# Performance work log

Measured on AMD Instinct MI355X. Metric: run time of the kernel, lower is better.

The kernel has to match this reference:

```python
import jax, jax.numpy as jnp
import numpy as np

B, T, C_EMB, HEAD = 8, 2048, 1024, 64

def setup_inputs() -> dict:
    key = jax.random.key(0)
    kx, kq, kk, kv = jax.random.split(key, 4)
    x = jax.random.normal(kx, (B, T, C_EMB), dtype=jnp.float32)
    s = 1.0 / np.sqrt(C_EMB)
    Wq = jax.random.normal(kq, (C_EMB, HEAD), dtype=jnp.float32) * s
    Wk = jax.random.normal(kk, (C_EMB, HEAD), dtype=jnp.float32) * s
    Wv = jax.random.normal(kv, (C_EMB, HEAD), dtype=jnp.float32) * s
    return {"x": x, "Wq": Wq, "Wk": Wk, "Wv": Wv}


def _apply_rotary(q, k):
    # q, k: [B, T, D] with D = head_size; matches torch apply_rotary_emb
    D = q.shape[-1]
    pos = jnp.arange(q.shape[1], dtype=jnp.float32)                # [T]
    dim_arr = jnp.arange(0, D, 2, dtype=jnp.float32)               # [D/2]
    freqs = 10000.0 ** (-dim_arr / D)                              # [D/2]
    theta = pos[:, None] * freqs[None, :]                          # [T, D/2]
    cos = jnp.concatenate([jnp.cos(theta), jnp.cos(theta)], -1)[None]  # [1,T,D]
    sin = jnp.concatenate([jnp.sin(theta), jnp.sin(theta)], -1)[None]

    def rot(v):
        v1, v2 = v[..., : D // 2], v[..., D // 2 :]
        return jnp.concatenate([-v2, v1], axis=-1)

    return q * cos + rot(q) * sin, k * cos + rot(k) * sin


def reference(x, Wq, Wk, Wv):
    Bx, Tx, Cx = x.shape
    q = x @ Wq  # [B,T,H]
    k = x @ Wk
    v = x @ Wv
    q, k = _apply_rotary(q, k)
    # NOTE: original scales by C**-0.5 where C = n_embd, not head_size
    scale = Cx ** (-0.5)
    wei = jnp.einsum("bqd,bkd->bqk", q, k) * scale                 # [B,T,T]
    causal = jnp.tril(jnp.ones((Tx, Tx), dtype=bool))
    wei = jnp.where(causal[None], wei, -jnp.inf)
    wei = jax.nn.softmax(wei, axis=-1)
    out = jnp.einsum("bqk,bkd->bqd", wei, v)                       # [B,T,H]
    return out
```

## Files before the change

kernel.cpp:

```cpp
#include <hip/hip_runtime.h>

typedef __bf16 bf16x8 __attribute__((ext_vector_type(8)));
typedef float f32x4 __attribute__((ext_vector_type(4)));
typedef unsigned short u16;

#define MFMA __builtin_amdgcn_mfma_f32_16x16x32_bf16

__device__ __forceinline__ u16 f2bf_bits(float f) {
  unsigned u = __builtin_bit_cast(unsigned, f);
  u = (u + 0x7fffu + ((u >> 16) & 1u)) >> 16;
  return (u16)u;
}
__device__ __forceinline__ __bf16 f2bf(float f) {
  u16 b = f2bf_bits(f);
  return __builtin_bit_cast(__bf16, b);
}
__device__ __forceinline__ float bf2f(u16 b) {
  return __builtin_bit_cast(float, (unsigned)b << 16);
}

__device__ __forceinline__ int swz_off(int row, int col) {
  return row * 64 + ((((col >> 3) ^ row) & 7) << 3) + (col & 7);
}
__device__ __forceinline__ bf16x8 lds_read8(const __bf16* buf, int row, int col) {
  return *(const bf16x8*)(buf + (row * 64 + ((((col >> 3) ^ row) & 7) << 3)));
}
__device__ __forceinline__ void lds_write8(__bf16* buf, int row, int col, bf16x8 v) {
  *(bf16x8*)(buf + (row * 64 + ((((col >> 3) ^ row) & 7) << 3))) = v;
}

__global__ __launch_bounds__(256) void prep_w_kernel(
    const float* __restrict__ Wq, const float* __restrict__ Wk,
    const float* __restrict__ Wv, u16* __restrict__ wtg) {
  int idx = blockIdx.x * 256 + threadIdx.x;
  if (idx >= 192 * 1024) return;
  int row = idx >> 10, k = idx & 1023;
  const float* W = (row < 64) ? Wq : ((row < 128) ? Wk : Wv);
  int col = row & 63;
  wtg[idx] = f2bf_bits(W[(size_t)k * 64 + col]);
}

__device__ __forceinline__ void rope2(f32x4& lo, f32x4& hi, int i, float t_base) {
  float f = __expf(-(float)i * 0.28782313662425572f);
  const float inv2pi = 0.15915494309189535f;
#pragma unroll
  for (int r = 0; r < 4; ++r) {
    float rev = (t_base + (float)r) * f * inv2pi;
    rev = __builtin_amdgcn_fractf(rev);
    float sn = __builtin_amdgcn_sinf(rev);
    float cs = __builtin_amdgcn_cosf(rev);
    float L = lo[r], H = hi[r];
    lo[r] = L * cs - H * sn;
    hi[r] = H * cs + L * sn;
  }
}

__global__ __launch_bounds__(512) void qkv_rope_kernel(
    const float* __restrict__ x, const u16* __restrict__ wtg,
    u16* __restrict__ qg, u16* __restrict__ kg, u16* __restrict__ vtg) {
  __shared__ __bf16 xbuf[2][64 * 64];
  __shared__ __bf16 wbuf[2][192 * 64];
  const int tid = threadIdx.x;
  const int w = tid >> 6, l = tid & 63;
  const int wrg = w & 1;
  const int wcg = w >> 1;
  const int lr = l & 15, lg = l >> 4;
  const int r0 = blockIdx.x * 64;
  const int b = r0 >> 11, t0 = r0 & 2047;
  constexpr int TM4[4][3] = {{0, 2, 8}, {1, 3, 9}, {4, 6, 10}, {5, 7, 11}};

  f32x4 acc[2][3];
#pragma unroll
  for (int rg = 0; rg < 2; ++rg)
#pragma unroll
    for (int j = 0; j < 3; ++j) acc[rg][j] = (f32x4){0.f, 0.f, 0.f, 0.f};

  const int srow = tid >> 3, sc8 = tid & 7;
  const float* xbase = x + (size_t)(r0 + srow) * 1024 + sc8 * 8;

  float4 xA0, xA1, xB0, xB1;
  bf16x8 swr[3];

  auto loadW = [&](int k0) {
#pragma unroll
    for (int s = 0; s < 3; ++s) {
      int id = tid + s * 512;
      swr[s] = *(const bf16x8*)(wtg + (size_t)(id >> 3) * 1024 + k0 + (id & 7) * 8);
    }
  };
  auto writeW = [&](int bsel) {
#pragma unroll
    for (int s = 0; s < 3; ++s) {
      int id = tid + s * 512;
      lds_write8(wbuf[bsel], id >> 3, (id & 7) * 8, swr[s]);
    }
  };
  auto writeX = [&](int bsel, float4 a0, float4 a1) {
    bf16x8 v;
    v[0] = f2bf(a0.x); v[1] = f2bf(a0.y); v[2] = f2bf(a0.z); v[3] = f2bf(a0.w);
    v[4] = f2bf(a1.x); v[5] = f2bf(a1.y); v[6] = f2bf(a1.z); v[7] = f2bf(a1.w);
    lds_write8(xbuf[bsel], srow, sc8 * 8, v);
  };

  xA0 = *(const float4*)xbase;
  xA1 = *(const float4*)(xbase + 4);
  loadW(0);
  writeX(0, xA0, xA1);
  writeW(0);
  xB0 = *(const float4*)(xbase + 64);
  xB1 = *(const float4*)(xbase + 68);
  __syncthreads();

#pragma unroll
  for (int s = 0; s < 16; ++s) {
    const int cur = s & 1;
    if (s < 14) {
      const float* p = xbase + (size_t)(s + 2) * 64;
      if (cur == 0) { xA0 = *(const float4*)p; xA1 = *(const float4*)(p + 4); }
      else          { xB0 = *(const float4*)p; xB1 = *(const float4*)(p + 4); }
    }
    if (s < 15) loadW((s + 1) * 64);
#pragma unroll
    for (int kk = 0; kk < 2; ++kk) {
      bf16x8 a0 = lds_read8(xbuf[cur], wrg * 32 + lr, kk * 32 + lg * 8);
      bf16x8 a1 = lds_read8(xbuf[cur], wrg * 32 + 16 + lr, kk * 32 + lg * 8);
#pragma unroll
      for (int j = 0; j < 3; ++j) {
        bf16x8 bb = lds_read8(wbuf[cur], TM4[wcg][j] * 16 + lr, kk * 32 + lg * 8);
        acc[0][j] = MFMA(a0, bb, acc[0][j], 0, 0, 0);
        acc[1][j] = MFMA(a1, bb, acc[1][j], 0, 0, 0);
      }
    }
    if (s < 15) {
      if (cur == 0) writeX(1, xB0, xB1);
      else          writeX(0, xA0, xA1);
      writeW(cur ^ 1);
      __syncthreads();
    }
  }

  const int ph = (wcg & 1) * 16 + lr;
#pragma unroll
  for (int rg = 0; rg < 2; ++rg) {
    const int rowb = wrg * 32 + rg * 16 + lg * 4;
    const float t_base = (float)(t0 + rowb);
    rope2(acc[rg][0], acc[rg][1], ph, t_base);
    if (wcg < 2) {
#pragma unroll
      for (int r = 0; r < 4; ++r) {
        size_t rowo = (size_t)(r0 + rowb + r) * 64;
        qg[rowo + ph] = f2bf_bits(acc[rg][0][r] * 0.03125f);
        qg[rowo + 32 + ph] = f2bf_bits(acc[rg][1][r] * 0.03125f);
      }
    } else {
#pragma unroll
      for (int r = 0; r < 4; ++r) {
        size_t rowo = (size_t)(r0 + rowb + r) * 64;
        kg[rowo + ph] = f2bf_bits(acc[rg][0][r]);
        kg[rowo + 32 + ph] = f2bf_bits(acc[rg][1][r]);
      }
    }
    {
      const int d = (TM4[wcg][2] - 8) * 16 + lr;
      ushort4 uv;
      uv.x = f2bf_bits(acc[rg][2][0]);
      uv.y = f2bf_bits(acc[rg][2][1]);
      uv.z = f2bf_bits(acc[rg][2][2]);
      uv.w = f2bf_bits(acc[rg][2][3]);
      *(ushort4*)(vtg + (size_t)(b * 64 + d) * 2048 + t0 + rowb) = uv;
    }
  }
}

__global__ __launch_bounds__(256) void attn_part_kernel(
    const u16* __restrict__ qg, const u16* __restrict__ kg,
    const u16* __restrict__ vtg, u16* __restrict__ opart,
    float* __restrict__ lpart, float* __restrict__ out, int CT, int NCH) {
  const int idx = blockIdx.x;
  const int b = idx / (32 * NCH);
  const int rem = idx % (32 * NCH);
  const int qt = rem / NCH, ch = rem % NCH;
  const int t0v = ch * CT;
  if (t0v > qt) return;
  const int t1v = min(qt + 1, t0v + CT);
  const int nv = qt / CT + 1;

  __shared__ __bf16 kbuf[2][64 * 64];
  __shared__ __bf16 vbuf[2][64 * 64];
  __shared__ __bf16 pbuf[4 * 16 * 64];
  const int tid = threadIdx.x;
  const int w = tid >> 6, l = tid & 63;
  const int lr = l & 15, lg = l >> 4;
  const int q0 = qt * 64;
  const float NEG_INF = -__builtin_inff();

  const u16* qrow = qg + (size_t)(b * 2048 + q0 + w * 16 + lr) * 64;
  bf16x8 qf0 = *(const bf16x8*)(qrow + lg * 8);
  bf16x8 qf1 = *(const bf16x8*)(qrow + 32 + lg * 8);

  bf16x8 kr[2], vr[2];
  auto stage_load = [&](int c) {
#pragma unroll
    for (int s = 0; s < 2; ++s) {
      int id = tid + s * 256;
      int row = id >> 3, c8 = id & 7;
      kr[s] = *(const bf16x8*)(kg + (size_t)(b * 2048 + c * 64 + row) * 64 + c8 * 8);
      vr[s] = *(const bf16x8*)(vtg + (size_t)(b * 64 + row) * 2048 + c * 64 + c8 * 8);
    }
  };
  auto stage_write = [&](int bsel) {
#pragma unroll
    for (int s = 0; s < 2; ++s) {
      int id = tid + s * 256;
      int row = id >> 3, c8 = id & 7;
      lds_write8(kbuf[bsel], row, c8 * 8, kr[s]);
      lds_write8(vbuf[bsel], row, c8 * 8, vr[s]);
    }
  };

  f32x4 acc_o[4];
#pragma unroll
  for (int n = 0; n < 4; ++n) acc_o[n] = (f32x4){0.f, 0.f, 0.f, 0.f};
  float l_p[4] = {0.f, 0.f, 0.f, 0.f};

  stage_load(t0v);
  stage_write(0);
  __syncthreads();

  for (int c = t0v; c < t1v; ++c) {
    const int cur = (c - t0v) & 1;
    const bool more = (c + 1 < t1v);
    if (more) stage_load(c + 1);

    f32x4 s4[4];
#pragma unroll
    for (int nt = 0; nt < 4; ++nt) {
      bf16x8 k0 = lds_read8(kbuf[cur], nt * 16 + lr, lg * 8);
      bf16x8 k1 = lds_read8(kbuf[cur], nt * 16 + lr, 32 + lg * 8);
      f32x4 t = (f32x4){0.f, 0.f, 0.f, 0.f};
      t = MFMA(qf0, k0, t, 0, 0, 0);
      t = MFMA(qf1, k1, t, 0, 0, 0);
      s4[nt] = t;
    }
    if (c == qt) {
#pragma unroll
      for (int nt = 0; nt < 4; ++nt)
#pragma unroll
        for (int r = 0; r < 4; ++r) {
          int kv = nt * 16 + lr, qq = w * 16 + lg * 4 + r;
          if (kv > qq) s4[nt][r] = NEG_INF;
        }
    }
    __bf16* pw = pbuf + w * (16 * 64);
#pragma unroll
    for (int nt = 0; nt < 4; ++nt)
#pragma unroll
      for (int r = 0; r < 4; ++r) {
        float p = __expf(s4[nt][r] - 8.0f);
        l_p[r] += p;
        pw[swz_off(lg * 4 + r, nt * 16 + lr)] = f2bf(p);
      }
#pragma unroll
    for (int h = 0; h < 2; ++h) {
      bf16x8 pf = lds_read8(pw, lr, h * 32 + lg * 8);
#pragma unroll
      for (int nt = 0; nt < 4; ++nt) {
        bf16x8 vf = lds_read8(vbuf[cur], nt * 16 + lr, h * 32 + lg * 8);
        acc_o[nt] = MFMA(pf, vf, acc_o[nt], 0, 0, 0);
      }
    }
    if (more) {
      stage_write(cur ^ 1);
      __syncthreads();
    }
  }

  float lsum[4];
#pragma unroll
  for (int r = 0; r < 4; ++r) {
    float s = l_p[r];
    s += __shfl_xor(s, 1);
    s += __shfl_xor(s, 2);
    s += __shfl_xor(s, 4);
    s += __shfl_xor(s, 8);
    lsum[r] = s;
  }

  if (nv == 1) {
#pragma unroll
    for (int r = 0; r < 4; ++r) {
      float inv = 1.0f / lsum[r];
      size_t rowo = (size_t)(b * 2048 + q0 + w * 16 + lg * 4 + r) * 64;
#pragma unroll
      for (int nt = 0; nt < 4; ++nt)
        out[rowo + nt * 16 + lr] = acc_o[nt][r] * inv;
    }
    return;
  }

  const size_t slot = (size_t)(b * 32 + qt) * NCH + ch;
  u16* oslot = opart + slot * 4096;
#pragma unroll
  for (int r = 0; r < 4; ++r) {
    int row = w * 16 + lg * 4 + r;
#pragma unroll
    for (int nt = 0; nt < 4; ++nt)
      oslot[row * 64 + nt * 16 + lr] = f2bf_bits(acc_o[nt][r]);
    if (lr == 0) lpart[slot * 64 + row] = lsum[r];
  }
}

__global__ __launch_bounds__(256) void attn_combine_kernel(
    const u16* __restrict__ opart, const float* __restrict__ lpart,
    float* __restrict__ out, int CT, int NCH) {
  const int bq = blockIdx.x >> 2;
  const int quarter = blockIdx.x & 3;
  const int b = bq >> 5, qt = bq & 31;
  const int nv = qt / CT + 1;
  if (nv == 1) return;
  const int row = quarter * 16 + (threadIdx.x >> 4);
  const int col = (threadIdx.x & 15) * 4;
  const size_t slot0 = (size_t)(b * 32 + qt) * NCH;

  float denom = 0.f;
  float acc[4] = {0.f, 0.f, 0.f, 0.f};
  for (int c = 0; c < nv; ++c) {
    denom += lpart[(slot0 + c) * 64 + row];
    ushort4 pv = *(const ushort4*)(opart + (slot0 + c) * 4096 + row * 64 + col);
    acc[0] += bf2f(pv.x);
    acc[1] += bf2f(pv.y);
    acc[2] += bf2f(pv.z);
    acc[3] += bf2f(pv.w);
  }
  float inv = 1.0f / denom;
  float4 o;
  o.x = acc[0] * inv; o.y = acc[1] * inv; o.z = acc[2] * inv; o.w = acc[3] * inv;
  *(float4*)(out + ((size_t)(b * 2048 + qt * 64 + row)) * 64 + col) = o;
}

extern "C" void kernel_launch(void* const* d_in, const int* in_sizes, int n_in,
                              void* d_out, int out_size, void* d_ws, size_t ws_size,
                              hipStream_t stream) {
  const float* x = (const float*)d_in[0];
  const float* Wq = (const float*)d_in[1];
  const float* Wk = (const float*)d_in[2];
  const float* Wv = (const float*)d_in[3];
  float* out = (float*)d_out;
  char* ws = (char*)d_ws;
  u16* wtg = (u16*)ws;
  u16* qg = (u16*)(ws + 393216);
  u16* kg = (u16*)(ws + 393216 + 2097152);
  u16* vtg = (u16*)(ws + 393216 + 2u * 2097152);
  const size_t base = 393216 + 3u * 2097152;
  int NCH = 8;
  while (NCH > 1 && base + (size_t)256 * NCH * 8448 > ws_size) NCH >>= 1;
  const int CT = 32 / NCH;
  u16* opart = (u16*)(ws + base);
  float* lpart = (float*)(ws + base + (size_t)256 * NCH * 8192);

  prep_w_kernel<<<dim3(768), dim3(256), 0, stream>>>(Wq, Wk, Wv, wtg);
  qkv_rope_kernel<<<dim3(256), dim3(512), 0, stream>>>(x, wtg, qg, kg, vtg);
  attn_part_kernel<<<dim3(8 * 32 * NCH), dim3(256), 0, stream>>>(
      qg, kg, vtg, opart, lpart, out, CT, NCH);
  attn_combine_kernel<<<dim3(256 * 4), dim3(256), 0, stream>>>(opart, lpart, out, CT, NCH);
}
```

Baseline: 53.22 us.

## Prefetch K/V two chunks ahead and transpose weights via shared-memory tile

The attention partial kernel now keeps two register sets of K/V staging data, so global loads for chunk c+2 are issued while chunk c is computed and chunk c+1 is written to LDS. This is meant to hide more global-load latency behind the MFMA work. Separately, the weight prep kernel transposes W through a padded shared tile, making both its reads and writes coalesced, and runs on 48 blocks instead of 768. The cost is extra VGPR pressure from the doubled staging registers, and with CT of 4 the deeper prefetch has few iterations to pay off.

```diff
diff --git a/kernel.cpp b/kernel.cpp
--- a/kernel.cpp
+++ b/kernel.cpp
@@ -32,12 +32,23 @@
 __global__ __launch_bounds__(256) void prep_w_kernel(
     const float* __restrict__ Wq, const float* __restrict__ Wk,
     const float* __restrict__ Wv, u16* __restrict__ wtg) {
-  int idx = blockIdx.x * 256 + threadIdx.x;
-  if (idx >= 192 * 1024) return;
-  int row = idx >> 10, k = idx & 1023;
-  const float* W = (row < 64) ? Wq : ((row < 128) ? Wk : Wv);
-  int col = row & 63;
-  wtg[idx] = f2bf_bits(W[(size_t)k * 64 + col]);
+  __shared__ float tile[64][65];
+  const int tid = threadIdx.x;
+  const int kt = blockIdx.x & 15;
+  const int ct = blockIdx.x >> 4;
+  const float* W = (ct == 0) ? Wq : ((ct == 1) ? Wk : Wv);
+  const int k0 = kt * 64;
+#pragma unroll
+  for (int i = 0; i < 16; ++i) {
+    int row = i * 4 + (tid >> 6), col = tid & 63;
+    tile[row][col] = W[(size_t)(k0 + row) * 64 + col];
+  }
+  __syncthreads();
+#pragma unroll
+  for (int i = 0; i < 16; ++i) {
+    int col = i * 4 + (tid >> 6), krow = tid & 63;
+    wtg[(size_t)(ct * 64 + col) * 1024 + k0 + krow] = f2bf_bits(tile[krow][col]);
+  }
 }
 
 __device__ __forceinline__ void rope2(f32x4& lo, f32x4& hi, int i, float t_base) {
@@ -198,23 +209,41 @@
   bf16x8 qf0 = *(const bf16x8*)(qrow + lg * 8);
   bf16x8 qf1 = *(const bf16x8*)(qrow + 32 + lg * 8);
 
-  bf16x8 kr[2], vr[2];
-  auto stage_load = [&](int c) {
+  const int srow = tid >> 3, sc8 = (tid & 7) * 8;
+  const u16* kgb = kg + (size_t)(b * 2048) * 64;
+  const u16* vtb = vtg + (size_t)(b * 64) * 2048;
+
+  bf16x8 krA[2], vrA[2], krB[2], vrB[2];
+  auto loadA = [&](int c) {
 #pragma unroll
     for (int s = 0; s < 2; ++s) {
-      int id = tid + s * 256;
-      int row = id >> 3, c8 = id & 7;
-      kr[s] = *(const bf16x8*)(kg + (size_t)(b * 2048 + c * 64 + row) * 64 + c8 * 8);
-      vr[s] = *(const bf16x8*)(vtg + (size_t)(b * 64 + row) * 2048 + c * 64 + c8 * 8);
-    }
-  };
-  auto stage_write = [&](int bsel) {
+      int row = srow + s * 32;
+      krA[s] = *(const bf16x8*)(kgb + (size_t)(c * 64 + row) * 64 + sc8);
+      vrA[s] = *(const bf16x8*)(vtb + (size_t)row * 2048 + c * 64 + sc8);
+    }
+  };
+  auto loadB = [&](int c) {
 #pragma unroll
     for (int s = 0; s < 2; ++s) {
-      int id = tid + s * 256;
-      int row = id >> 3, c8 = id & 7;
-      lds_write8(kbuf[bsel], row, c8 * 8, kr[s]);
-      lds_write8(vbuf[bsel], row, c8 * 8, vr[s]);
+      int row = srow + s * 32;
+      krB[s] = *(const bf16x8*)(kgb + (size_t)(c * 64 + row) * 64 + sc8);
+      vrB[s] = *(const bf16x8*)(vtb + (size_t)row * 2048 + c * 64 + sc8);
+    }
+  };
+  auto writeA = [&](int bsel) {
+#pragma unroll
+    for (int s = 0; s < 2; ++s) {
+      int row = srow + s * 32;
+      lds_write8(kbuf[bsel], row, sc8, krA[s]);
+      lds_write8(vbuf[bsel], row, sc8, vrA[s]);
+    }
+  };
+  auto writeB = [&](int bsel) {
+#pragma unroll
+    for (int s = 0; s < 2; ++s) {
+      int row = srow + s * 32;
+      lds_write8(kbuf[bsel], row, sc8, krB[s]);
+      lds_write8(vbuf[bsel], row, sc8, vrB[s]);
     }
   };
 
@@ -223,14 +252,17 @@
   for (int n = 0; n < 4; ++n) acc_o[n] = (f32x4){0.f, 0.f, 0.f, 0.f};
   float l_p[4] = {0.f, 0.f, 0.f, 0.f};
 
-  stage_load(t0v);
-  stage_write(0);
+  loadA(t0v);
+  writeA(0);
+  if (t0v + 1 < t1v) loadB(t0v + 1);
   __syncthreads();
 
   for (int c = t0v; c < t1v; ++c) {
     const int cur = (c - t0v) & 1;
-    const bool more = (c + 1 < t1v);
-    if (more) stage_load(c + 1);
+    if (c + 2 < t1v) {
+      if (cur == 0) loadA(c + 2);
+      else          loadB(c + 2);
+    }
 
     f32x4 s4[4];
 #pragma unroll
@@ -269,8 +301,9 @@
         acc_o[nt] = MFMA(pf, vf, acc_o[nt], 0, 0, 0);
       }
     }
-    if (more) {
-      stage_write(cur ^ 1);
+    if (c + 1 < t1v) {
+      if (cur == 0) writeB(1);
+      else          writeA(0);
       __syncthreads();
     }
   }
@@ -358,7 +391,7 @@
   u16* opart = (u16*)(ws + base);
   float* lpart = (float*)(ws + base + (size_t)256 * NCH * 8192);
 
-  prep_w_kernel<<<dim3(768), dim3(256), 0, stream>>>(Wq, Wk, Wv, wtg);
+  prep_w_kernel<<<dim3(48), dim3(256), 0, stream>>>(Wq, Wk, Wv, wtg);
   qkv_rope_kernel<<<dim3(256), dim3(512), 0, stream>>>(x, wtg, qg, kg, vtg);
   attn_part_kernel<<<dim3(8 * 32 * NCH), dim3(256), 0, stream>>>(
       qg, kg, vtg, opart, lpart, out, CT, NCH);
```

Result: slower. 55.98 us (+5.2%).
